# Kernel optimization log

Measured on AMD Instinct MI355X. Metric: run time of the kernel, lower is better.

The kernel has to match this reference:

```python
import jax, jax.numpy as jnp
import numpy as np

B = 16384
F_CAT = 26
CARD = 100000
F_NUM = 13
D = 16


def setup_inputs() -> dict:
    key = jax.random.key(0)
    ks = jax.random.split(key, 7)
    categorical_X = jax.random.randint(ks[0], (B, F_CAT), 0, CARD, dtype=jnp.int64 if jax.config.jax_enable_x64 else jnp.int32)
    numerical_X = jax.random.normal(ks[1], (B, F_NUM), dtype=jnp.float32)
    # Stacked per-field tables (equivalent to one nnx.Embed per field)
    Wc = jax.random.normal(ks[2], (F_CAT, CARD, D), dtype=jnp.float32) * 0.05  # 2nd-order categorical factors
    bc = jax.random.normal(ks[3], (F_CAT, CARD, 1), dtype=jnp.float32) * 0.05  # 1st-order categorical biases
    Wn = jax.random.normal(ks[4], (F_NUM, D), dtype=jnp.float32) * 0.05        # numerical factors (num_embeddings=1)
    bn = jax.random.normal(ks[5], (F_NUM, 1), dtype=jnp.float32) * 0.05        # numerical biases (num_embeddings=1)
    b0 = jax.random.normal(ks[6], (1,), dtype=jnp.float32)
    return {"categorical_X": categorical_X, "numerical_X": numerical_X,
            "Wc": Wc, "bc": bc, "Wn": Wn, "bn": bn, "b0": b0}


def reference(categorical_X, numerical_X, Wc, bc, Wn, bn, b0):
    f_idx = jnp.arange(F_CAT)[None, :]                      # [1, F]
    # Per-field gathers: V rows for each feature
    Vc = Wc[f_idx, categorical_X]                           # [B, F, D]
    Vn = Wn[None, :, :] * numerical_X[:, :, None]           # [B, Fn, D]
    V = jnp.concatenate([Vc, Vn], axis=1)                   # [B, F+Fn, D]
    # FM sum-square trick: (||sum_i v_i||^2 - sum_i ||v_i||^2) / 2
    s = V.sum(axis=1)                                       # [B, D]
    interaction = 0.5 * ((s * s).sum(axis=-1) - (V * V).sum(axis=(1, 2)))  # [B]
    # Bias (1st-order) term
    bias = bc[f_idx, categorical_X, 0].sum(axis=1) + (numerical_X * bn[None, :, 0]).sum(axis=1) + b0[0]  # [B]
    return (bias + interaction).reshape(-1, 1)              # [B, 1]
```

## Files before the change

### kernel.cpp

```cpp
#include <hip/hip_runtime.h>

constexpr int B     = 16384;
constexpr int F_CAT = 26;
constexpr int CARD  = 100000;
constexpr int F_NUM = 13;
constexpr int D     = 16;

__global__ __launch_bounds__(256) void fm_fwd(
    const int*   __restrict__ cat,
    const float* __restrict__ num,
    const float* __restrict__ Wc,
    const float* __restrict__ bc,
    const float* __restrict__ Wn,
    const float* __restrict__ bn,
    const float* __restrict__ b0,
    float*       __restrict__ out)
{
    const int tid = blockIdx.x * blockDim.x + threadIdx.x;
    const int row = tid >> 2;
    const int sub = tid & 3;
    if (row >= B) return;

    int idx[F_CAT];
    {
        const int* cp = cat + row * F_CAT;
#pragma unroll
        for (int q = 0; q < 6; ++q) {
            const int4 v = *reinterpret_cast<const int4*>(cp + q * 4);
            idx[q * 4 + 0] = v.x; idx[q * 4 + 1] = v.y;
            idx[q * 4 + 2] = v.z; idx[q * 4 + 3] = v.w;
        }
        const int2 t = *reinterpret_cast<const int2*>(cp + 24);
        idx[24] = t.x; idx[25] = t.y;
    }

    float acc = 0.f;
#pragma unroll
    for (int f = sub; f < F_CAT; f += 4) {
        acc += bc[(size_t)f * CARD + (size_t)idx[f]];
    }

    float4 s = make_float4(0.f, 0.f, 0.f, 0.f);
    float ssq = 0.f;

#pragma unroll
    for (int f = 0; f < F_CAT; ++f) {
        const float4 v = *reinterpret_cast<const float4*>(
            Wc + ((size_t)f * CARD + (size_t)idx[f]) * D + sub * 4);
        s.x += v.x; s.y += v.y; s.z += v.z; s.w += v.w;
        ssq += v.x * v.x + v.y * v.y + v.z * v.z + v.w * v.w;
    }

#pragma unroll
    for (int i = 0; i < F_NUM; ++i) {
        const float x = num[row * F_NUM + i];
        const float4 w = *reinterpret_cast<const float4*>(Wn + i * D + sub * 4);
        s.x += x * w.x; s.y += x * w.y; s.z += x * w.z; s.w += x * w.w;
        ssq += x * x * (w.x * w.x + w.y * w.y + w.z * w.z + w.w * w.w);
    }
#pragma unroll
    for (int i = sub; i < F_NUM; i += 4) {
        acc += num[row * F_NUM + i] * bn[i];
    }

    float part = 0.5f * (s.x * s.x + s.y * s.y + s.z * s.z + s.w * s.w - ssq) + acc;
    part += __shfl_xor(part, 1);
    part += __shfl_xor(part, 2);

    if (sub == 0) out[row] = part + b0[0];
}

extern "C" void kernel_launch(void* const* d_in, const int* in_sizes, int n_in,
                              void* d_out, int out_size, void* d_ws, size_t ws_size,
                              hipStream_t stream) {
    const int*   cat = (const int*)  d_in[0];
    const float* num = (const float*)d_in[1];
    const float* Wc  = (const float*)d_in[2];
    const float* bc  = (const float*)d_in[3];
    const float* Wn  = (const float*)d_in[4];
    const float* bn  = (const float*)d_in[5];
    const float* b0  = (const float*)d_in[6];
    float*       out = (float*)d_out;

    const int threads = B * 4;
    const int block   = 256;
    const int grid    = (threads + block - 1) / block;
    fm_fwd<<<grid, block, 0, stream>>>(cat, num, Wc, bc, Wn, bn, b0, out);
}
```

Before: 228.8 us.

## Split each row across 32 threads: fields halved, one scalar dim per lane

Each batch row is now handled by 32 lanes instead of 4. The 26 categorical fields are split into two halves of 13, and each lane loads a single float of the 16-wide embedding rather than a float4. Partial sums are combined with a cross-half shuffle followed by a 32-lane butterfly reduction. This gives more memory-level parallelism for the random gathers and more waves in flight, at the cost of scalar loads, redundant index loads per lane, and more shuffle work.

After: 227.0 us, median of 2. About the same (-0.8%).

```diff
diff --git a/kernel.cpp b/kernel.cpp
--- a/kernel.cpp
+++ b/kernel.cpp
@@ -16,58 +16,53 @@
     const float* __restrict__ b0,
     float*       __restrict__ out)
 {
-    const int tid = blockIdx.x * blockDim.x + threadIdx.x;
-    const int row = tid >> 2;
-    const int sub = tid & 3;
-    if (row >= B) return;
+    const int tid  = blockIdx.x * blockDim.x + threadIdx.x;
+    const int row  = tid >> 5;
+    const int l32  = tid & 31;
+    const int half = l32 >> 4;
+    const int d    = l32 & 15;
 
-    int idx[F_CAT];
-    {
-        const int* cp = cat + row * F_CAT;
+    const int fbase = half * 13;
+    const int* rowc = cat + row * F_CAT + fbase;
+
+    int idx[13];
 #pragma unroll
-        for (int q = 0; q < 6; ++q) {
-            const int4 v = *reinterpret_cast<const int4*>(cp + q * 4);
-            idx[q * 4 + 0] = v.x; idx[q * 4 + 1] = v.y;
-            idx[q * 4 + 2] = v.z; idx[q * 4 + 3] = v.w;
-        }
-        const int2 t = *reinterpret_cast<const int2*>(cp + 24);
-        idx[24] = t.x; idx[25] = t.y;
+    for (int i = 0; i < 13; ++i) idx[i] = rowc[i];
+
+    float acc = 0.f;
+    if (d < 13) acc = bc[(size_t)(fbase + d) * CARD + (size_t)idx[d]];
+
+    float v[13];
+#pragma unroll
+    for (int i = 0; i < 13; ++i) {
+        v[i] = Wc[((size_t)(fbase + i) * CARD + (size_t)idx[i]) * D + d];
     }
 
-    float acc = 0.f;
+    float s = 0.f, ssq = 0.f;
 #pragma unroll
-    for (int f = sub; f < F_CAT; f += 4) {
-        acc += bc[(size_t)f * CARD + (size_t)idx[f]];
+    for (int i = 0; i < 13; ++i) { s += v[i]; ssq += v[i] * v[i]; }
+
+    if (half == 0) {
+        const float* nr = num + row * F_NUM;
+#pragma unroll
+        for (int i = 0; i < F_NUM; ++i) {
+            const float x  = nr[i];
+            const float vx = x * Wn[i * D + d];
+            s += vx; ssq += vx * vx;
+        }
+    } else if (d < 13) {
+        acc += num[row * F_NUM + d] * bn[d];
     }
 
-    float4 s = make_float4(0.f, 0.f, 0.f, 0.f);
-    float ssq = 0.f;
+    const float s_full = s + __shfl_xor(s, 16);
+    float t = 0.25f * s_full * s_full - 0.5f * ssq + acc;
+    t += __shfl_xor(t, 1);
+    t += __shfl_xor(t, 2);
+    t += __shfl_xor(t, 4);
+    t += __shfl_xor(t, 8);
+    t += __shfl_xor(t, 16);
 
-#pragma unroll
-    for (int f = 0; f < F_CAT; ++f) {
-        const float4 v = *reinterpret_cast<const float4*>(
-            Wc + ((size_t)f * CARD + (size_t)idx[f]) * D + sub * 4);
-        s.x += v.x; s.y += v.y; s.z += v.z; s.w += v.w;
-        ssq += v.x * v.x + v.y * v.y + v.z * v.z + v.w * v.w;
-    }
-
-#pragma unroll
-    for (int i = 0; i < F_NUM; ++i) {
-        const float x = num[row * F_NUM + i];
-        const float4 w = *reinterpret_cast<const float4*>(Wn + i * D + sub * 4);
-        s.x += x * w.x; s.y += x * w.y; s.z += x * w.z; s.w += x * w.w;
-        ssq += x * x * (w.x * w.x + w.y * w.y + w.z * w.z + w.w * w.w);
-    }
-#pragma unroll
-    for (int i = sub; i < F_NUM; i += 4) {
-        acc += num[row * F_NUM + i] * bn[i];
-    }
-
-    float part = 0.5f * (s.x * s.x + s.y * s.y + s.z * s.z + s.w * s.w - ssq) + acc;
-    part += __shfl_xor(part, 1);
-    part += __shfl_xor(part, 2);
-
-    if (sub == 0) out[row] = part + b0[0];
+    if (l32 == 0) out[row] = t + b0[0];
 }
 
 extern "C" void kernel_launch(void* const* d_in, const int* in_sizes, int n_in,
@@ -82,8 +77,8 @@
     const float* b0  = (const float*)d_in[6];
     float*       out = (float*)d_out;
 
-    const int threads = B * 4;
+    const int threads = B * 32;
     const int block   = 256;
-    const int grid    = (threads + block - 1) / block;
+    const int grid    = threads / block;
     fm_fwd<<<grid, block, 0, stream>>>(cat, num, Wc, bc, Wn, bn, b0, out);
 }
```
